# Optimization experiments

Measured on AMD Instinct MI355X. Metric: run time of the kernel, lower is better.

## Reference

```python
import jax, jax.numpy as jnp
import numpy as np

H, W, S = 480, 1024, 32
MULT_THRESH, ADD_THRESH = 0.01, 0.1


def setup_inputs() -> dict:
    key = jax.random.key(0)
    k1, k2 = jax.random.split(key)
    flows_f = jax.random.normal(k1, (1, S, 2, H, W), jnp.float32)
    noise = jax.random.normal(k2, (1, S, 2, H, W), jnp.float32)
    # near-inverse backward flow so the fwd-bwd consistency check passes for many points
    flows_b = -flows_f + 0.05 * noise
    return {"flows_f": flows_f, "flows_b": flows_b, "margin": 10, "sample_step": 4}


def bilinear_sample(im, x, y):
    # im: (C,H,W); x,y: (N,) float pixel coords -> (C,N). Matches torch bilinear_sample2d
    # (weights from unclipped coords, gather indices clipped to the image).
    C, Hh, Ww = im.shape
    x0 = jnp.floor(x); y0 = jnp.floor(y)
    wx1 = x - x0; wx0 = 1.0 - wx1
    wy1 = y - y0; wy0 = 1.0 - wy1
    x0i = jnp.clip(x0.astype(jnp.int32), 0, Ww - 1)
    x1i = jnp.clip(x0i + 1, 0, Ww - 1)
    y0i = jnp.clip(y0.astype(jnp.int32), 0, Hh - 1)
    y1i = jnp.clip(y0i + 1, 0, Hh - 1)
    g = lambda yi, xi: im[:, yi, xi]  # (C,N)
    return (g(y0i, x0i) * (wy0 * wx0) + g(y0i, x1i) * (wy0 * wx1)
            + g(y1i, x0i) * (wy1 * wx0) + g(y1i, x1i) * (wy1 * wx1))


def _forward(ff, fb, margin, sample_step):
    # ff, fb: (S, 2, H, W) forward / backward flows (batch squeezed, B=1)
    gy = jnp.arange(margin, H - margin + 1, sample_step, dtype=jnp.float32)
    gx = jnp.arange(margin, W - margin + 1, sample_step, dtype=jnp.float32)
    YY, XX = jnp.meshgrid(gy, gx, indexing='ij')
    ys_g = YY.reshape(-1); xs_g = XX.reshape(-1)          # (G,) base sampling grid
    G = xs_g.shape[0]
    N = 2 * H * W // (sample_step ** 2)                   # trajectory slot capacity
    R = min(N, G)                                         # max births per step (static)

    by, bx = jnp.meshgrid(jnp.arange(H, dtype=jnp.float32),
                          jnp.arange(W, dtype=jnp.float32), indexing='ij')

    def prune(flow_f, flow_b):
        # fwd-bwd consistency mask 'on': (H,W) in {0,1}
        xt = (bx + flow_f[0]).reshape(-1)
        yt = (by + flow_f[1]).reshape(-1)
        fbw = bilinear_sample(flow_b, xt, yt).reshape(2, H, W)  # backwarped bwd flow
        diff = jnp.sqrt(jnp.sum((flow_f + fbw) ** 2, axis=0))
        mag = 0.5 * (jnp.sqrt(jnp.sum(flow_f ** 2, axis=0)) + jnp.sqrt(jnp.sum(fbw ** 2, axis=0)))
        return (diff <= MULT_THRESH * mag + ADD_THRESH).astype(jnp.float32)

    X = jnp.zeros((S, N), jnp.float32)
    Y = jnp.zeros((S, N), jnp.float32)
    Start = -jnp.ones((N,), jnp.float32)
    X = X.at[0, :G].set(xs_g)
    Y = Y.at[0, :G].set(ys_g)
    Start = Start.at[:G].set(0.0)

    def step(carry, inp):
        X, Y, Start = carry
        flow_f, flow_b, s = inp
        on = prune(flow_f, flow_b)                         # (H,W)
        active = Start >= 0.0                              # (N,) live-slot mask (replaces where(Start>=0))
        xs_o = X[s]; ys_o = Y[s]
        uv = bilinear_sample(flow_f, xs_o, ys_o)           # (2,N) flow at current points
        xs_t = xs_o + uv[0]; ys_t = ys_o + uv[1]
        fb_ok = bilinear_sample(on[None], xs_o, ys_o)[0] > 0.5
        marg = ((xs_t > margin) & (ys_t > margin) &
                (xs_t < W - margin) & (ys_t < H - margin))
        choose = active & marg & fb_ok
        # scatter surviving points into row s+1 (row starts as zeros, matching init)
        X = X.at[s + 1].set(jnp.where(choose, xs_t, 0.0))
        Y = Y.at[s + 1].set(jnp.where(choose, ys_t, 0.0))
        Start = jnp.where(active & ~choose, -1.0, Start)   # terminated slots freed
        # occupancy map of surviving targets, dilated by 5x5 ones-conv (== maxpool on binary)
        oy = jnp.where(choose, ys_t, jnp.float32(H)).astype(jnp.int32)
        ox = jnp.where(choose, xs_t, jnp.float32(W)).astype(jnp.int32)
        occ = jnp.zeros((H, W), jnp.float32).at[oy, ox].set(1.0, mode='drop')
        occ = jax.lax.reduce_window(occ, 0.0, jax.lax.max, (5, 5), (1, 1), 'SAME')
        map_occ = bilinear_sample(occ[None], xs_g, ys_g)[0]
        free_cand = (1.0 - map_occ) == 1.0                 # (G,) unoccupied grid points
        # compaction without dynamic shapes: stable-sort free-first, keep original order
        cand_order = jnp.argsort(~free_cand, stable=True)  # free candidates first
        num_cand = jnp.sum(free_cand)
        free_slot = Start < 0.0
        slot_order = jnp.argsort(~free_slot, stable=True)  # free slots first
        num_free = jnp.sum(free_slot)
        m = jnp.minimum(num_cand, num_free)
        r = jnp.arange(R)
        tgt = jnp.where(r < m, slot_order[:R], N)          # index N -> dropped
        X = X.at[s + 1, tgt].set(xs_g[cand_order[:R]], mode='drop')
        Y = Y.at[s + 1, tgt].set(ys_g[cand_order[:R]], mode='drop')
        Start = Start.at[tgt].set((s + 1).astype(jnp.float32), mode='drop')
        return (X, Y, Start), None

    steps = jnp.arange(S - 1)
    (X, Y, Start), _ = jax.lax.scan(step, (X, Y, Start), (ff[:-1], fb[:-1], steps))
    return jnp.stack([X, Y]), Start


def reference(flows_f, flows_b, margin, sample_step):
    # Returns dense trajectory buffers XY: (2, S, N) and final Start: (N,)
    # (the ragged python-list trajectory extraction is a host-side post-process).
    return _forward(flows_f[0], flows_b[0], margin, sample_step)
```

## Files before the change

### kernel.cpp

```cpp
#include <hip/hip_runtime.h>
#include <cstdint>

#define HH 480
#define WW 1024
#define SS 32
#define HW (HH*WW)
#define MARGIN 10
#define STEP 4
#define GYC 116
#define GXC 252
#define GG (GYC*GXC)
#define NSLOT (2*HH*WW/(STEP*STEP))
#define NBLK (NSLOT/256)
#define CW ((GG+63)/64)
#define CWP 512
#define FPW 256
#define CPB 122

__device__ __forceinline__ unsigned long long aload64(const unsigned long long* p) {
  return __hip_atomic_load(p, __ATOMIC_RELAXED, __HIP_MEMORY_SCOPE_AGENT);
}
__device__ __forceinline__ void astore64(unsigned long long* p, unsigned long long v) {
  __hip_atomic_store(p, v, __ATOMIC_RELAXED, __HIP_MEMORY_SCOPE_AGENT);
}
__device__ __forceinline__ void aor64(unsigned long long* p, unsigned long long v) {
  (void)__hip_atomic_fetch_or(p, v, __ATOMIC_RELAXED, __HIP_MEMORY_SCOPE_AGENT);
}

__device__ __forceinline__ int clampi(int v, int lo, int hi) {
  return v < lo ? lo : (v > hi ? hi : v);
}

__device__ __forceinline__ void ld2(const float* __restrict__ base, int row, int xlo,
                                    float& c0, float& c1) {
  int bx = (xlo < WW - 1) ? xlo : (WW - 2);
  float2 v;
  __builtin_memcpy(&v, base + row * WW + bx, 8);
  c0 = (xlo == bx) ? v.x : v.y;
  c1 = v.y;
}

__global__ __launch_bounds__(256) void k_init(unsigned long long* __restrict__ flags,
                                              unsigned int* __restrict__ bmp32)
{
  int idx = blockIdx.x * 256 + threadIdx.x;
  if (idx < 32 * CWP * 2) bmp32[idx] = 0u;
  if (idx < 256) {
    unsigned long long v = (idx < NBLK) ? 0ull : (0x7FFFFFFFull << 32);
    flags[idx] = v;
    flags[FPW + idx] = v;
  }
}

struct Bil {
  int x0i, x1i, y0i, y1i;
  int i00, i01, i10, i11;
  float w00, w01, w10, w11;
};

__device__ __forceinline__ Bil mkbil(float xs, float ys) {
#pragma clang fp contract(off)
  float x0 = floorf(xs), y0 = floorf(ys);
  float wx1 = xs - x0, wx0 = 1.0f - wx1;
  float wy1 = ys - y0, wy0 = 1.0f - wy1;
  Bil b;
  b.x0i = clampi((int)x0, 0, WW - 1);
  b.x1i = b.x0i + 1 > WW - 1 ? WW - 1 : b.x0i + 1;
  b.y0i = clampi((int)y0, 0, HH - 1);
  b.y1i = b.y0i + 1 > HH - 1 ? HH - 1 : b.y0i + 1;
  b.i00 = b.y0i * WW + b.x0i; b.i01 = b.y0i * WW + b.x1i;
  b.i10 = b.y1i * WW + b.x0i; b.i11 = b.y1i * WW + b.x1i;
  b.w00 = wy0 * wx0; b.w01 = wy0 * wx1;
  b.w10 = wy1 * wx0; b.w11 = wy1 * wx1;
  return b;
}

__device__ __forceinline__ float prune_val(float fx, float fy,
    float c00a, float c01a, float c10a, float c11a,
    float c00b, float c01b, float c10b, float c11b, const Bil& t)
{
#pragma clang fp contract(off)
  float bw0 = ((c00a * t.w00 + c01a * t.w01) + c10a * t.w10) + c11a * t.w11;
  float bw1 = ((c00b * t.w00 + c01b * t.w01) + c10b * t.w10) + c11b * t.w11;
  float t0 = fx + bw0, t1 = fy + bw1;
  float diff = sqrtf(t0 * t0 + t1 * t1);
  float magf = sqrtf(fx * fx + fy * fy);
  float magb = sqrtf(bw0 * bw0 + bw1 * bw1);
  float mag = 0.5f * (magf + magb);
  return (diff <= 0.01f * mag + 0.1f) ? 1.0f : 0.0f;
}

__device__ __forceinline__ unsigned long long make_intadv(
    int pix, int piy, float fx, float fy, const float* __restrict__ bks)
{
#pragma clang fp contract(off)
  float xt = (float)pix + fx, yt = (float)piy + fy;
  Bil Bt = mkbil(xt, yt);
  const float* b0p = bks;
  const float* b1p = bks + HW;
  float o = prune_val(fx, fy,
                      b0p[Bt.i00], b0p[Bt.i01], b0p[Bt.i10], b0p[Bt.i11],
                      b1p[Bt.i00], b1p[Bt.i01], b1p[Bt.i10], b1p[Bt.i11], Bt);
  bool marg = (xt > (float)MARGIN) && (yt > (float)MARGIN) &&
              (xt < (float)(WW - MARGIN)) && (yt < (float)(HH - MARGIN));
  bool ch = marg && (o > 0.5f);
  unsigned lo = __float_as_uint(ch ? xt : 0.0f);
  unsigned hi = __float_as_uint(ch ? yt : -1.0f);
  return ((unsigned long long)hi << 32) | (unsigned long long)lo;
}

__global__ __launch_bounds__(256, 1) void k_steps(
    const float* __restrict__ ff, const float* __restrict__ fbk,
    float* __restrict__ X, float* __restrict__ Y, float* __restrict__ Start,
    unsigned long long* __restrict__ bmp, unsigned long long* __restrict__ flags,
    unsigned long long* __restrict__ intadv)
{
#pragma clang fp contract(off)
  const int b = blockIdx.x;
  const int lane = threadIdx.x & 63;
  const int wv = threadIdx.x >> 6;
  const int slot = ((wv * NBLK + b) << 6) | lane;
  const unsigned long long ltmask = (1ull << lane) - 1ull;

  __shared__ unsigned long long wds[CWP];
  __shared__ unsigned int pref[CWP];
  __shared__ int wsum[4];
  __shared__ int wcnt[2][4];
  __shared__ int ps4[4];

  float x = 0.f, y = 0.f, st = -1.f;
  int mode = 0;
  float pf0 = 0.f, pf1 = 0.f, pf2 = 0.f, pf3 = 0.f;
  float pf4 = 0.f, pf5 = 0.f, pf6 = 0.f, pf7 = 0.f;
  float pb[32];
  float pxt = 0.f, pyt = 0.f;
  bool  pmarg = false;
  unsigned long long pa64 = (unsigned long long)0xBF800000u << 32;

  const int pj = threadIdx.x >> 1;
  const int pcell = b * CPB + pj;
  const bool prod = ((threadIdx.x & 1) == 0) && (pj < CPB) && (pcell < GG);
  int pix = 0, piy = 0, pp = 0;
  float fNx = 0.f, fNy = 0.f;
  float fCx = 0.f, fCy = 0.f;
  float bC0 = 0.f, bC1 = 0.f, bC2 = 0.f, bC3 = 0.f;
  float bC4 = 0.f, bC5 = 0.f, bC6 = 0.f, bC7 = 0.f;

  if (slot < GG) {
    int ii = slot / GXC, jj = slot - ii * GXC;
    int ix = MARGIN + STEP * jj, iy = MARGIN + STEP * ii;
    x = (float)ix; y = (float)iy;
    st = 0.f; mode = 2;
    int p0_ = iy * WW + ix;
    float f0x = ff[p0_], f0y = ff[HW + p0_];
    pa64 = make_intadv(ix, iy, f0x, f0y, fbk);
  }
  X[slot] = x; Y[slot] = y;

  if (prod) {
    int ii = pcell / GXC, jj = pcell - ii * GXC;
    pix = MARGIN + STEP * jj; piy = MARGIN + STEP * ii;
    pp = piy * WW + pix;
    float f1x = ff[(size_t)1 * 2 * HW + pp], f1y = ff[(size_t)1 * 2 * HW + HW + pp];
    float f2x = ff[(size_t)2 * 2 * HW + pp], f2y = ff[(size_t)2 * 2 * HW + HW + pp];
    float f3x = ff[(size_t)3 * 2 * HW + pp], f3y = ff[(size_t)3 * 2 * HW + HW + pp];
    fNx = ff[(size_t)4 * 2 * HW + pp];       fNy = ff[(size_t)4 * 2 * HW + HW + pp];
    astore64(&intadv[(size_t)1 * GG + pcell],
             make_intadv(pix, piy, f1x, f1y, fbk + (size_t)1 * 2 * HW));
    astore64(&intadv[(size_t)2 * GG + pcell],
             make_intadv(pix, piy, f2x, f2y, fbk + (size_t)2 * 2 * HW));
    {
      float xt = (float)pix + f3x, yt = (float)piy + f3y;
      Bil Bt = mkbil(xt, yt);
      const float* bb0 = fbk + (size_t)3 * 2 * HW;
      const float* bb1 = bb0 + HW;
      ld2(bb0, Bt.y0i, Bt.x0i, bC0, bC1);
      ld2(bb0, Bt.y1i, Bt.x0i, bC2, bC3);
      ld2(bb1, Bt.y0i, Bt.x0i, bC4, bC5);
      ld2(bb1, Bt.y1i, Bt.x0i, bC6, bC7);
      fCx = f3x; fCy = f3y;
    }
  }

#define ISSUE_TAP(tt, TXI, TYI, FX, FY) do { \
    Bil Bt = mkbil((float)P.TXI + (FX), (float)P.TYI + (FY)); \
    ld2(b0n, Bt.y0i, Bt.x0i, pb[(tt)*8+0], pb[(tt)*8+1]); \
    ld2(b0n, Bt.y1i, Bt.x0i, pb[(tt)*8+2], pb[(tt)*8+3]); \
    ld2(b1n, Bt.y0i, Bt.x0i, pb[(tt)*8+4], pb[(tt)*8+5]); \
    ld2(b1n, Bt.y1i, Bt.x0i, pb[(tt)*8+6], pb[(tt)*8+7]); \
  } while (0)

#define PRUNE_TAP(tt, TXI, TYI, FX, FY, OUT) do { \
    Bil Bt = mkbil((float)P.TXI + (FX), (float)P.TYI + (FY)); \
    OUT = prune_val((FX), (FY), \
                    pb[(tt)*8+0], pb[(tt)*8+1], pb[(tt)*8+2], pb[(tt)*8+3], \
                    pb[(tt)*8+4], pb[(tt)*8+5], pb[(tt)*8+6], pb[(tt)*8+7], Bt); \
  } while (0)

  for (int s = 0; s < SS - 1; ++s) {
    unsigned long long* pl = bmp + (size_t)(s + 1) * CWP;

    bool moved = false;
    if (mode == 1) {
      Bil P = mkbil(x, y);
      float o0, o1, o2, o3;
      PRUNE_TAP(0, x0i, y0i, pf0, pf4, o0);
      PRUNE_TAP(1, x1i, y0i, pf1, pf5, o1);
      PRUNE_TAP(2, x0i, y1i, pf2, pf6, o2);
      PRUNE_TAP(3, x1i, y1i, pf3, pf7, o3);
      float fbv = ((o0 * P.w00 + o1 * P.w01) + o2 * P.w10) + o3 * P.w11;
      if (pmarg && fbv > 0.5f) {
        x = pxt; y = pyt;
        moved = true;
      } else { st = -1.f; x = 0.f; y = 0.f; mode = 0; }
    } else if (mode == 2) {
      float axt = __uint_as_float((unsigned)pa64);
      float ayt = __uint_as_float((unsigned)(pa64 >> 32));
      if (ayt >= 0.0f) {
        x = axt; y = ayt; mode = 1;
        moved = true;
      } else { st = -1.f; x = 0.f; y = 0.f; mode = 0; }
    }
    if (moved) {
      int oy = (int)y, ox = (int)x;
      int i0 = ((oy - (MARGIN + 2) + 4099) >> 2) - 1024;
      int i1 = ((oy - (MARGIN - 2) + 4096) >> 2) - 1024;
      int j0 = ((ox - (MARGIN + 2) + 4099) >> 2) - 1024;
      int j1 = ((ox - (MARGIN - 2) + 4096) >> 2) - 1024;
      if (i0 < 0) i0 = 0; if (i1 > GYC - 1) i1 = GYC - 1;
      if (j0 < 0) j0 = 0; if (j1 > GXC - 1) j1 = GXC - 1;
      for (int i = i0; i <= i1; ++i) {
        int g0 = i * GXC + j0;
        int w = g0 >> 6, bo = g0 & 63;
        unsigned long long m = ((j1 > j0) ? 3ull : 1ull) << bo;
        aor64(&pl[w], m);
        if (bo == 63 && j1 > j0) aor64(&pl[w + 1], 1ull);
      }
    }
    unsigned long long smask = __ballot(st < 0.0f);
    if (lane == 0) wcnt[s & 1][wv] = (int)__popcll(smask);

    unsigned long long* fb = flags + (s & 1) * FPW;
    const int epoch = s + 1;
    __syncthreads();
    if (threadIdx.x == 0) {
      const int* wc = wcnt[s & 1];
      unsigned cpack = (unsigned)wc[0] | ((unsigned)wc[1] << 8)
                     | ((unsigned)wc[2] << 16) | ((unsigned)wc[3] << 24);
      astore64(&fb[b],
               ((unsigned long long)(unsigned)epoch << 32) | (unsigned long long)cpack);
    }

    if (mode == 1 && s < SS - 2) {
      const float* f0n = ff + (size_t)(s + 1) * 2 * HW;
      const float* f1n = f0n + HW;
      Bil P = mkbil(x, y);
      ld2(f0n, P.y0i, P.x0i, pf0, pf1);
      ld2(f0n, P.y1i, P.x0i, pf2, pf3);
      ld2(f1n, P.y0i, P.x0i, pf4, pf5);
      ld2(f1n, P.y1i, P.x0i, pf6, pf7);
      float u_ = ((pf0 * P.w00 + pf1 * P.w01) + pf2 * P.w10) + pf3 * P.w11;
      float v_ = ((pf4 * P.w00 + pf5 * P.w01) + pf6 * P.w10) + pf7 * P.w11;
      pxt = x + u_; pyt = y + v_;
      pmarg = (pxt > (float)MARGIN) && (pyt > (float)MARGIN) &&
              (pxt < (float)(WW - MARGIN)) && (pyt < (float)(HH - MARGIN));
      const float* b0n = fbk + (size_t)(s + 1) * 2 * HW;
      const float* b1n = b0n + HW;
      ISSUE_TAP(0, x0i, y0i, pf0, pf4);
      ISSUE_TAP(1, x1i, y0i, pf1, pf5);
      ISSUE_TAP(2, x0i, y1i, pf2, pf6);
      ISSUE_TAP(3, x1i, y1i, pf3, pf7);
    }
    if (prod) {
      if (s <= SS - 5) {
        float xt = (float)pix + fCx, yt = (float)piy + fCy;
        Bil Bt = mkbil(xt, yt);
        float o = prune_val(fCx, fCy, bC0, bC1, bC2, bC3, bC4, bC5, bC6, bC7, Bt);
        bool marg = (xt > (float)MARGIN) && (yt > (float)MARGIN) &&
                    (xt < (float)(WW - MARGIN)) && (yt < (float)(HH - MARGIN));
        bool ch = marg && (o > 0.5f);
        unsigned lo = __float_as_uint(ch ? xt : 0.0f);
        unsigned hi = __float_as_uint(ch ? yt : -1.0f);
        astore64(&intadv[(size_t)(s + 3) * GG + pcell],
                 ((unsigned long long)hi << 32) | (unsigned long long)lo);
      }
      if (s <= SS - 6) {
        float xt = (float)pix + fNx, yt = (float)piy + fNy;
        Bil Bt = mkbil(xt, yt);
        const float* bb0 = fbk + (size_t)(s + 4) * 2 * HW;
        const float* bb1 = bb0 + HW;
        ld2(bb0, Bt.y0i, Bt.x0i, bC0, bC1);
        ld2(bb0, Bt.y1i, Bt.x0i, bC2, bC3);
        ld2(bb1, Bt.y0i, Bt.x0i, bC4, bC5);
        ld2(bb1, Bt.y1i, Bt.x0i, bC6, bC7);
        fCx = fNx; fCy = fNy;
      }
      if (s <= SS - 7) {
        const float* fp_ = ff + (size_t)(s + 5) * 2 * HW;
        fNx = fp_[pp]; fNy = fp_[HW + pp];
      }
    }

    if (threadIdx.x < 64) {
      unsigned long long v0, v1, v2, v3;
      for (;;) {
        v0 = aload64(&fb[lane      ]);
        v1 = aload64(&fb[lane +  64]);
        v2 = aload64(&fb[lane + 128]);
        v3 = aload64(&fb[lane + 192]);
        unsigned m0 = (unsigned)(v0 >> 32), m1 = (unsigned)(v1 >> 32);
        unsigned m2 = (unsigned)(v2 >> 32), m3 = (unsigned)(v3 >> 32);
        unsigned mn = m0 < m1 ? m0 : m1;
        unsigned mn2 = m2 < m3 ? m2 : m3;
        mn = mn < mn2 ? mn : mn2;
        for (int o = 32; o > 0; o >>= 1) {
          unsigned t = (unsigned)__shfl_xor((int)mn, o, 64);
          mn = mn < t ? mn : t;
        }
        if ((int)mn >= epoch) break;
        __builtin_amdgcn_s_sleep(1);
      }
      auto up = [](unsigned long long f) -> unsigned long long {
        unsigned c = (unsigned)f;
        return (unsigned long long)(c & 0xFFu)
             | ((unsigned long long)((c >>  8) & 0xFFu) << 16)
             | ((unsigned long long)((c >> 16) & 0xFFu) << 32)
             | ((unsigned long long)((c >> 24) & 0xFFu) << 48);
      };
      unsigned long long u0 = up(v0), u1 = up(v1), u2 = up(v2), u3 = up(v3);
      unsigned long long F = u0 + u1 + u2 + u3;
      unsigned long long Pp = (lane       < b ? u0 : 0ull)
                            + (lane +  64 < b ? u1 : 0ull)
                            + (lane + 128 < b ? u2 : 0ull)
                            + (lane + 192 < b ? u3 : 0ull);
      for (int o = 32; o > 0; o >>= 1) {
        unsigned flo = (unsigned)F, fhi = (unsigned)(F >> 32);
        unsigned plo = (unsigned)Pp, phi = (unsigned)(Pp >> 32);
        unsigned flo2 = (unsigned)__shfl_xor((int)flo, o, 64);
        unsigned fhi2 = (unsigned)__shfl_xor((int)fhi, o, 64);
        unsigned plo2 = (unsigned)__shfl_xor((int)plo, o, 64);
        unsigned phi2 = (unsigned)__shfl_xor((int)phi, o, 64);
        F  += ((unsigned long long)fhi2 << 32) | flo2;
        Pp += ((unsigned long long)phi2 << 32) | plo2;
      }
      if (lane == 0) {
        int f0 = (int)(F & 0xFFFF), f1 = (int)((F >> 16) & 0xFFFF), f2 = (int)((F >> 32) & 0xFFFF);
        int p0 = (int)(Pp & 0xFFFF), p1 = (int)((Pp >> 16) & 0xFFFF);
        int p2 = (int)((Pp >> 32) & 0xFFFF), p3 = (int)((Pp >> 48) & 0xFFFF);
        ps4[0] = p0;
        ps4[1] = f0 + p1;
        ps4[2] = f0 + f1 + p2;
        ps4[3] = f0 + f1 + f2 + p3;
      }
    }
    __syncthreads();
    int ps = ps4[wv];

    {
      int t = threadIdx.x;
      int e0 = 2 * t, e1 = 2 * t + 1;
      unsigned long long m0 = 0ull, m1 = 0ull;
      if (e0 < CW) m0 = ~aload64(&pl[e0]);
      if (e1 < CW) m1 = ~aload64(&pl[e1]);
      if (e0 == CW - 1) m0 &= (1ull << 48) - 1ull;
      if (e1 == CW - 1) m1 &= (1ull << 48) - 1ull;
      wds[e0] = m0; wds[e1] = m1;
      int p0 = __popcll(m0), p1 = __popcll(m1);
      int v = p0 + p1;
      for (int o = 1; o < 64; o <<= 1) {
        int uu = __shfl_up(v, o, 64);
        if (lane >= o) v += uu;
      }
      if (lane == 63) wsum[wv] = v;
      __syncthreads();
      int base = 0;
      for (int j2 = 0; j2 < wv; ++j2) base += wsum[j2];
      pref[e0] = (unsigned int)(base + v - p1);
      pref[e1] = (unsigned int)(base + v);
      __syncthreads();
    }
    int tc = (int)pref[CWP - 1];

    if (st < 0.0f) {
      int r = ps + (int)__popcll(smask & ltmask);
      if (r < tc) {
        int k = 0;
        for (int bb = 256; bb >= 1; bb >>= 1) {
          int nk = k + bb;
          if (nk <= CWP - 1 && (int)pref[nk - 1] <= r) k = nk;
        }
        int j = r - (k ? (int)pref[k - 1] : 0);
        unsigned long long m = wds[k];
        int lo = 0;
        for (int bb = 32; bb >= 1; bb >>= 1) {
          int nb2 = lo + bb;
          unsigned long long mask = (nb2 >= 64) ? ~0ull : ((1ull << nb2) - 1ull);
          if (__popcll(m & mask) <= j) lo = nb2;
        }
        int g = k * 64 + lo;
        int ii = g / GXC, jj = g - ii * GXC;
        x = (float)(MARGIN + STEP * jj);
        y = (float)(MARGIN + STEP * ii);
        st = (float)(s + 1);
        mode = 2;
        if (s < SS - 2)
          pa64 = aload64(&intadv[(size_t)(s + 1) * GG + g]);
      }
    }
    X[(size_t)(s + 1) * NSLOT + slot] = x;
    Y[(size_t)(s + 1) * NSLOT + slot] = y;
  }

#undef ISSUE_TAP
#undef PRUNE_TAP

  Start[slot] = st;
}

extern "C" void kernel_launch(void* const* d_in, const int* in_sizes, int n_in,
                              void* d_out, int out_size, void* d_ws, size_t ws_size,
                              hipStream_t stream) {
  const float* ff  = (const float*)d_in[0];
  const float* fbk = (const float*)d_in[1];

  float* X     = (float*)d_out;
  float* Y     = X + (size_t)SS * NSLOT;
  float* Start = Y + (size_t)SS * NSLOT;

  unsigned long long* flags  = (unsigned long long*)d_ws;
  unsigned long long* bmp    = flags + 2 * FPW;
  unsigned long long* intadv = bmp + 32 * CWP;

  k_init<<<128, 256, 0, stream>>>(flags, (unsigned int*)bmp);

  k_steps<<<NBLK, 256, 0, stream>>>(ff, fbk, X, Y, Start, bmp, flags, intadv);
}
```

Before: 385.4 us.

## Let every wave poll grid flags and defer stores to overlap latency

All four waves now spin on the inter-block flag array and compute their own prefix offset with a wave-wide all-vote. This removes the shared-memory broadcast and one __syncthreads per step. The bilinear flow loads are split so their arithmetic and backward-tap issue happen after the producer work, which hides the load latency. X/Y stores are deferred by one step so they sit off the critical path before the spin-wait. In exchange, four times as many waves poll global memory, adding contention on the flag lines.

```diff
diff --git a/kernel.cpp b/kernel.cpp
--- a/kernel.cpp
+++ b/kernel.cpp
@@ -126,7 +126,6 @@
   __shared__ unsigned int pref[CWP];
   __shared__ int wsum[4];
   __shared__ int wcnt[2][4];
-  __shared__ int ps4[4];
 
   float x = 0.f, y = 0.f, st = -1.f;
   int mode = 0;
@@ -156,6 +155,7 @@
     pa64 = make_intadv(ix, iy, f0x, f0y, fbk);
   }
   X[slot] = x; Y[slot] = y;
+  float rx = x, ry = y;
 
   if (prod) {
     int ii = pcell / GXC, jj = pcell - ii * GXC;
@@ -251,25 +251,19 @@
                ((unsigned long long)(unsigned)epoch << 32) | (unsigned long long)cpack);
     }
 
-    if (mode == 1 && s < SS - 2) {
-      const float* f0n = ff + (size_t)(s + 1) * 2 * HW;
-      const float* f1n = f0n + HW;
-      Bil P = mkbil(x, y);
+    X[(size_t)s * NSLOT + slot] = rx;
+    Y[(size_t)s * NSLOT + slot] = ry;
+
+    const bool dopipe = (mode == 1 && s < SS - 2);
+    Bil P;
+    const float* f0n = ff + (size_t)(s + 1) * 2 * HW;
+    const float* f1n = f0n + HW;
+    if (dopipe) {
+      P = mkbil(x, y);
       ld2(f0n, P.y0i, P.x0i, pf0, pf1);
       ld2(f0n, P.y1i, P.x0i, pf2, pf3);
       ld2(f1n, P.y0i, P.x0i, pf4, pf5);
       ld2(f1n, P.y1i, P.x0i, pf6, pf7);
-      float u_ = ((pf0 * P.w00 + pf1 * P.w01) + pf2 * P.w10) + pf3 * P.w11;
-      float v_ = ((pf4 * P.w00 + pf5 * P.w01) + pf6 * P.w10) + pf7 * P.w11;
-      pxt = x + u_; pyt = y + v_;
-      pmarg = (pxt > (float)MARGIN) && (pyt > (float)MARGIN) &&
-              (pxt < (float)(WW - MARGIN)) && (pyt < (float)(HH - MARGIN));
-      const float* b0n = fbk + (size_t)(s + 1) * 2 * HW;
-      const float* b1n = b0n + HW;
-      ISSUE_TAP(0, x0i, y0i, pf0, pf4);
-      ISSUE_TAP(1, x1i, y0i, pf1, pf5);
-      ISSUE_TAP(2, x0i, y1i, pf2, pf6);
-      ISSUE_TAP(3, x1i, y1i, pf3, pf7);
     }
     if (prod) {
       if (s <= SS - 5) {
@@ -300,8 +294,22 @@
         fNx = fp_[pp]; fNy = fp_[HW + pp];
       }
     }
-
-    if (threadIdx.x < 64) {
+    if (dopipe) {
+      float u_ = ((pf0 * P.w00 + pf1 * P.w01) + pf2 * P.w10) + pf3 * P.w11;
+      float v_ = ((pf4 * P.w00 + pf5 * P.w01) + pf6 * P.w10) + pf7 * P.w11;
+      pxt = x + u_; pyt = y + v_;
+      pmarg = (pxt > (float)MARGIN) && (pyt > (float)MARGIN) &&
+              (pxt < (float)(WW - MARGIN)) && (pyt < (float)(HH - MARGIN));
+      const float* b0n = fbk + (size_t)(s + 1) * 2 * HW;
+      const float* b1n = b0n + HW;
+      ISSUE_TAP(0, x0i, y0i, pf0, pf4);
+      ISSUE_TAP(1, x1i, y0i, pf1, pf5);
+      ISSUE_TAP(2, x0i, y1i, pf2, pf6);
+      ISSUE_TAP(3, x1i, y1i, pf3, pf7);
+    }
+
+    int ps;
+    {
       unsigned long long v0, v1, v2, v3;
       for (;;) {
         v0 = aload64(&fb[lane      ]);
@@ -313,11 +321,7 @@
         unsigned mn = m0 < m1 ? m0 : m1;
         unsigned mn2 = m2 < m3 ? m2 : m3;
         mn = mn < mn2 ? mn : mn2;
-        for (int o = 32; o > 0; o >>= 1) {
-          unsigned t = (unsigned)__shfl_xor((int)mn, o, 64);
-          mn = mn < t ? mn : t;
-        }
-        if ((int)mn >= epoch) break;
+        if (__all((int)mn >= epoch)) break;
         __builtin_amdgcn_s_sleep(1);
       }
       auto up = [](unsigned long long f) -> unsigned long long {
@@ -343,18 +347,11 @@
         F  += ((unsigned long long)fhi2 << 32) | flo2;
         Pp += ((unsigned long long)phi2 << 32) | plo2;
       }
-      if (lane == 0) {
-        int f0 = (int)(F & 0xFFFF), f1 = (int)((F >> 16) & 0xFFFF), f2 = (int)((F >> 32) & 0xFFFF);
-        int p0 = (int)(Pp & 0xFFFF), p1 = (int)((Pp >> 16) & 0xFFFF);
-        int p2 = (int)((Pp >> 32) & 0xFFFF), p3 = (int)((Pp >> 48) & 0xFFFF);
-        ps4[0] = p0;
-        ps4[1] = f0 + p1;
-        ps4[2] = f0 + f1 + p2;
-        ps4[3] = f0 + f1 + f2 + p3;
-      }
-    }
-    __syncthreads();
-    int ps = ps4[wv];
+      int f0 = (int)(F & 0xFFFF), f1 = (int)((F >> 16) & 0xFFFF);
+      int f2 = (int)((F >> 32) & 0xFFFF);
+      int pw = (int)((Pp >> (16 * wv)) & 0xFFFF);
+      ps = pw + ((wv > 0) ? f0 : 0) + ((wv > 1) ? f1 : 0) + ((wv > 2) ? f2 : 0);
+    }
 
     {
       int t = threadIdx.x;
@@ -407,13 +404,14 @@
           pa64 = aload64(&intadv[(size_t)(s + 1) * GG + g]);
       }
     }
-    X[(size_t)(s + 1) * NSLOT + slot] = x;
-    Y[(size_t)(s + 1) * NSLOT + slot] = y;
+    rx = x; ry = y;
   }
 
 #undef ISSUE_TAP
 #undef PRUNE_TAP
 
+  X[(size_t)(SS - 1) * NSLOT + slot] = rx;
+  Y[(size_t)(SS - 1) * NSLOT + slot] = ry;
   Start[slot] = st;
 }
 
```

After: 392.8 us. About the same (+1.9%).
